# Performance work log

Hardware: AMD Instinct MI355X
Metric: run time of the kernel (lower is better)

## Reference

```python
import jax, jax.numpy as jnp
import numpy as np

B, S, H, F = 4, 1024, 768, 3072
EC, EU = 4, 4          # common / unique expert counts
CAP_FACTOR = 1.0       # common_ffn_capacity


def setup_inputs() -> dict:
    key = jax.random.key(0)
    ks = jax.random.split(key, 8)
    def w(k, shape, s=0.02):
        return jax.random.normal(k, shape, jnp.float32) * s
    return {
        "hidden_states": jax.random.normal(ks[0], (B, S, H), jnp.float32),
        "Wsc": w(ks[1], (H, EC)), "bsc": jnp.zeros((EC,), jnp.float32),
        "W1c": w(ks[2], (EC, H, F)), "b1c": jnp.zeros((EC, F), jnp.float32),
        "W2c": w(ks[3], (EC, F, H)), "b2c": jnp.zeros((EC, H), jnp.float32),
        "Wsu": w(ks[4], (H, EU)), "bsu": jnp.zeros((EU,), jnp.float32),
        "W1u": w(ks[5], (EU, H, F)), "b1u": jnp.zeros((EU, F), jnp.float32),
        "W2u": w(ks[6], (EU, F, H)), "b2u": jnp.zeros((EU, H), jnp.float32),
    }


def _ffn(x, W1, b1, W2, b2):
    # standard BERT FFN: dense -> exact GELU -> dense
    return jax.nn.gelu(x @ W1 + b1, approximate=False) @ W2 + b2


def _expert_mix(h, route, W1, b1, W2, b2, n_exp):
    # top-1 dispatch expressed as masked per-expert compute (loop over fixed small E)
    out = jnp.zeros_like(h)
    for e in range(n_exp):
        m = (route == e).astype(h.dtype)[:, None]
        out = out + m * _ffn(h, W1[e], b1[e], W2[e], b2[e])
    return out


def _drop_mask(route, pmax, capacity):
    # rank tokens within each expert group by router prob (descending);
    # tokens with rank >= capacity are 'dropped' (routed to unique experts)
    N = route.shape[0]
    order = jnp.lexsort((-jax.lax.stop_gradient(pmax), route))  # primary: expert id, secondary: -prob
    rs = route[order]
    starts = jnp.searchsorted(rs, rs, side='left')              # first index of each group
    rank_sorted = jnp.arange(N) - starts
    rank = jnp.zeros((N,), jnp.int32).at[order].set(rank_sorted.astype(jnp.int32))
    return rank >= capacity


def reference(hidden_states, Wsc, bsc, W1c, b1c, W2c, b2c, Wsu, bsu, W1u, b1u, W2u, b2u):
    shp = hidden_states.shape
    h = hidden_states.reshape(-1, shp[-1])          # [N, H]
    N = h.shape[0]
    capacity = int(CAP_FACTOR * N / EC)             # static python int

    # --- common routing (top-1 + capacity dropping) ---
    pc = jax.nn.softmax(h @ Wsc + bsc, axis=-1)
    pmax_c = jnp.max(pc, axis=-1)
    route_c = jnp.argmax(pc, axis=-1)
    dropped = _drop_mask(route_c, pmax_c, capacity)

    # NOTE: original code never truncates cluster_list, so common FFN runs on ALL tokens
    scale_c = (pmax_c / jax.lax.stop_gradient(pmax_c))[:, None]   # == 1.0, grad-carrying
    common = _expert_mix(h, route_c, W1c, b1c, W2c, b2c, EC) * scale_c

    # --- unique routing (only dropped tokens contribute) ---
    pu = jax.nn.softmax(h @ Wsu + bsu, axis=-1)
    pmax_u = jnp.max(pu, axis=-1)
    route_u = jnp.argmax(pu, axis=-1)
    scale_u = (pmax_u / jax.lax.stop_gradient(pmax_u))[:, None]
    unique = _expert_mix(h, route_u, W1u, b1u, W2u, b2u, EU) * scale_u

    # dropped tokens get common + unique; kept tokens get common only
    out = common + dropped[:, None].astype(h.dtype) * unique
    return out.reshape(shp)
```

## Files before the change

kernel.cpp:

```cpp
#include <hip/hip_runtime.h>
#include <hip/hip_bf16.h>
#include <math.h>

#define NTOK 4096
#define HDIM 768
#define FDIM 3072
#define NEXP 4
#define MAXU 3072
#define MAXT 64
#define NPOS (NTOK + MAXU)
#define RSTRIDE 76

typedef __attribute__((ext_vector_type(4))) float f32x4;
typedef __attribute__((ext_vector_type(8))) short s16x8;

__device__ __forceinline__ unsigned short f2bf(float f) {
    union { float f; unsigned int u; } v; v.f = f;
    unsigned int u = v.u;
    unsigned int r = (u + 0x7fffu + ((u >> 16) & 1u)) >> 16;
    return (unsigned short)r;
}

__device__ __forceinline__ void gload_lds16(const unsigned short* g, unsigned short* l) {
    __builtin_amdgcn_global_load_lds((const __attribute__((address_space(1))) void*)g,
                                     (__attribute__((address_space(3))) void*)l, 16, 0, 0);
}

__global__ void __launch_bounds__(256) route_kernel(
    const float* __restrict__ h, const float* __restrict__ Wsc, const float* __restrict__ bsc,
    const float* __restrict__ Wsu, const float* __restrict__ bsu,
    int* __restrict__ route_c, float* __restrict__ pmax_c,
    int* __restrict__ route_u, int* __restrict__ counts)
{
    if (blockIdx.x == 0 && threadIdx.x < 8) counts[threadIdx.x] = 0;
    int tok = blockIdx.x * 4 + (threadIdx.x >> 6);
    int lane = threadIdx.x & 63;
    const float* hr = h + (size_t)tok * HDIM;
    float ac[4] = {0.f,0.f,0.f,0.f}, au[4] = {0.f,0.f,0.f,0.f};
    for (int k = lane; k < HDIM; k += 64) {
        float x = hr[k];
        const float4 wc = *(const float4*)(Wsc + k * 4);
        const float4 wu = *(const float4*)(Wsu + k * 4);
        ac[0] += x * wc.x; ac[1] += x * wc.y; ac[2] += x * wc.z; ac[3] += x * wc.w;
        au[0] += x * wu.x; au[1] += x * wu.y; au[2] += x * wu.z; au[3] += x * wu.w;
    }
    #pragma unroll
    for (int off = 32; off > 0; off >>= 1) {
        #pragma unroll
        for (int j = 0; j < 4; ++j) {
            ac[j] += __shfl_xor(ac[j], off);
            au[j] += __shfl_xor(au[j], off);
        }
    }
    if (lane == 0) {
        float lc[4], lu[4];
        #pragma unroll
        for (int j = 0; j < 4; ++j) { lc[j] = ac[j] + bsc[j]; lu[j] = au[j] + bsu[j]; }
        int bc = 0; float mc = lc[0];
        #pragma unroll
        for (int j = 1; j < 4; ++j) if (lc[j] > mc) { mc = lc[j]; bc = j; }
        float dc = 0.f;
        #pragma unroll
        for (int j = 0; j < 4; ++j) dc += expf(lc[j] - mc);
        route_c[tok] = bc; pmax_c[tok] = 1.0f / dc;
        int bu = 0; float mu = lu[0];
        #pragma unroll
        for (int j = 1; j < 4; ++j) if (lu[j] > mu) { mu = lu[j]; bu = j; }
        route_u[tok] = bu;
    }
}

__global__ void __launch_bounds__(256) rank_kernel(
    const int* __restrict__ rc, const int* __restrict__ ru,
    const float* __restrict__ pc,
    int* __restrict__ dropped, int* __restrict__ counts, int capacity)
{
    int i = blockIdx.x, t = threadIdx.x;
    int e = rc[i]; float pi = pc[i];
    int cnt = 0;
    for (int j = t; j < NTOK; j += 256) {
        if (rc[j] == e) {
            float pj = pc[j];
            if (pj > pi || (pj == pi && j < i)) cnt++;
        }
    }
    __shared__ int red[256];
    red[t] = cnt; __syncthreads();
    for (int s = 128; s > 0; s >>= 1) {
        if (t < s) red[t] += red[t+s];
        __syncthreads();
    }
    if (t == 0) {
        int d = (red[0] >= capacity) ? 1 : 0;
        dropped[i] = d;
        atomicAdd(&counts[e], 1);
        if (d) atomicAdd(&counts[4 + ru[i]], 1);
    }
}

__global__ void offsets_kernel(const int* __restrict__ counts,
                               int* __restrict__ offAll,
                               int* __restrict__ cur,
                               int* __restrict__ tab,
                               int* __restrict__ ntot)
{
    if (threadIdx.x == 0 && blockIdx.x == 0) {
        int o = 0;
        for (int e = 0; e < 8; ++e) { offAll[e] = o; o += counts[e]; }
        offAll[8] = o;
        *ntot = o;
        for (int j = 0; j < 8; ++j) cur[j] = 0;
        int t = 0;
        for (int e = 0; e < 8; ++e) {
            int nt = (counts[e] + 127) >> 7;
            for (int m = 0; m < nt && t < MAXT; ++m) { tab[t*2] = e; tab[t*2+1] = m; ++t; }
        }
        for (; t < MAXT; ++t) { tab[t*2] = -1; tab[t*2+1] = 0; }
    }
}

__global__ void __launch_bounds__(256) scatter_kernel(
    const int* __restrict__ rc, const int* __restrict__ ru, const int* __restrict__ dropped,
    const int* __restrict__ offAll, int* __restrict__ cur, int* __restrict__ perm,
    int* __restrict__ invC, int* __restrict__ invU)
{
    int i = blockIdx.x * 256 + threadIdx.x;
    if (i >= NTOK) return;
    int e = rc[i];
    int p = offAll[e] + atomicAdd(&cur[e], 1);
    perm[p] = i;
    invC[i] = p;
    if (dropped[i]) {
        int eu = 4 + ru[i];
        int q = offAll[eu] + atomicAdd(&cur[eu], 1);
        perm[q] = i;
        invU[i] = q;
    }
}

__global__ void __launch_bounds__(192) gather_kernel(
    const float* __restrict__ h, const int* __restrict__ perm,
    const int* __restrict__ ntot, unsigned short* __restrict__ Xs)
{
    int pos = blockIdx.x;
    if (pos >= *ntot) return;
    int t = threadIdx.x;
    int tok = perm[pos];
    const float4 v = *(const float4*)(h + (size_t)tok * HDIM + t * 4);
    ushort4 o;
    o.x = f2bf(v.x); o.y = f2bf(v.y); o.z = f2bf(v.z); o.w = f2bf(v.w);
    *(ushort4*)(Xs + (size_t)pos * HDIM + t * 4) = o;
}

__global__ void __launch_bounds__(256) wtrans_kernel(
    const float* __restrict__ Wc, const float* __restrict__ Wu,
    unsigned short* __restrict__ Bt, int K, int N)
{
    int z = blockIdx.z;
    const float* We = (z < 4) ? (Wc + (size_t)z * K * N)
                              : (Wu + (size_t)(z - 4) * K * N);
    unsigned short* Be = Bt + (size_t)z * N * K;
    int k0 = blockIdx.y * 64, n0 = blockIdx.x * 64;
    __shared__ float t[64][65];
    int tid = threadIdx.x;
    int rr = tid >> 4, cc = (tid & 15) * 4;
    #pragma unroll
    for (int i = 0; i < 4; ++i) {
        int row = rr + i * 16;
        const float4 v = *(const float4*)(We + (size_t)(k0 + row) * N + n0 + cc);
        t[row][cc+0] = v.x; t[row][cc+1] = v.y; t[row][cc+2] = v.z; t[row][cc+3] = v.w;
    }
    __syncthreads();
    #pragma unroll
    for (int i = 0; i < 4; ++i) {
        int n = rr + i * 16;
        ushort4 o;
        o.x = f2bf(t[cc+0][n]); o.y = f2bf(t[cc+1][n]);
        o.z = f2bf(t[cc+2][n]); o.w = f2bf(t[cc+3][n]);
        *(ushort4*)(Be + (size_t)(n0 + n) * K + k0 + cc) = o;
    }
}

__global__ void __launch_bounds__(256, 4) ffn_gemm(
    const unsigned short* __restrict__ A, const unsigned short* __restrict__ Bt,
    const float* __restrict__ biasC, const float* __restrict__ biasU,
    const int* __restrict__ offs, const int* __restrict__ tab,
    unsigned short* __restrict__ Gout, float* __restrict__ Yout,
    int K, int N, int doGelu)
{
    int e = tab[blockIdx.y * 2];
    if (e < 0) return;
    int mt = tab[blockIdx.y * 2 + 1];
    int off = offs[e];
    int cnt = offs[e + 1] - off;
    if (mt * 128 >= cnt) return;
    int nt = blockIdx.x;
    int klen = K / gridDim.z;
    int kbeg = blockIdx.z * klen, kend = kbeg + klen;

    __shared__ unsigned short lds[9728];
    unsigned short* As = lds;
    unsigned short* Bs = lds + 4096;

    int tid = threadIdx.x;
    int lane = tid & 63, wave = tid >> 6;
    int quad = lane >> 4, l16 = lane & 15;

    f32x4 acc[2][4];
    #pragma unroll
    for (int a = 0; a < 2; ++a)
        #pragma unroll
        for (int b = 0; b < 4; ++b)
            acc[a][b] = (f32x4){0.f, 0.f, 0.f, 0.f};

    int r0 = tid >> 2, s0 = tid & 3;
    int r1 = (tid + 256) >> 2;
    int seg0 = (s0 ^ ((r0 & 3) ^ ((r0 >> 2) & 3))) * 8;
    int seg1 = (s0 ^ ((r1 & 3) ^ ((r1 >> 2) & 3))) * 8;
    int ar0 = mt * 128 + r0; if (ar0 >= cnt) ar0 = cnt - 1;
    int ar1 = mt * 128 + r1; if (ar1 >= cnt) ar1 = cnt - 1;

    const unsigned short* Ae = A + (size_t)off * K;
    const unsigned short* Be = Bt + ((size_t)e * N + (size_t)nt * 64) * K;
    const unsigned short* asrc0 = Ae + (size_t)ar0 * K + seg0;
    const unsigned short* asrc1 = Ae + (size_t)ar1 * K + seg1;
    const unsigned short* bsrc0 = Be + (size_t)r0 * K + seg0;
    unsigned short* al0 = &As[wave * 512];
    unsigned short* al1 = &As[2048 + wave * 512];
    unsigned short* bl0 = &Bs[wave * 512];
    int cca = quad ^ ((l16 & 3) ^ ((l16 >> 2) & 3));

    for (int k0 = kbeg; k0 < kend; k0 += 32) {
        gload_lds16(asrc0 + k0, al0);
        gload_lds16(asrc1 + k0, al1);
        gload_lds16(bsrc0 + k0, bl0);
        __syncthreads();

        s16x8 af[2], bf[4];
        #pragma unroll
        for (int mi = 0; mi < 2; ++mi)
            af[mi] = *(const s16x8*)&As[(wave * 32 + mi * 16 + l16) * 32 + cca * 8];
        #pragma unroll
        for (int ni = 0; ni < 4; ++ni)
            bf[ni] = *(const s16x8*)&Bs[(ni * 16 + l16) * 32 + cca * 8];
        #pragma unroll
        for (int mi = 0; mi < 2; ++mi)
            #pragma unroll
            for (int ni = 0; ni < 4; ++ni)
                acc[mi][ni] = __builtin_amdgcn_mfma_f32_16x16x32_bf16(af[mi], bf[ni], acc[mi][ni], 0, 0, 0);
        __syncthreads();
    }

    const float* bias = (e < 4) ? (biasC + (size_t)e * N) : (biasU + (size_t)(e - 4) * N);

    if (doGelu) {
        unsigned short* R = lds + wave * (32 * RSTRIDE);
        #pragma unroll
        for (int ni = 0; ni < 4; ++ni) {
            float bv = bias[nt * 64 + ni * 16 + l16];
            #pragma unroll
            for (int mi = 0; mi < 2; ++mi) {
                #pragma unroll
                for (int r = 0; r < 4; ++r) {
                    float x = acc[mi][ni][r] + bv;
                    x = 0.5f * x * (1.0f + erff(x * 0.70710678118654752440f));
                    R[(mi * 16 + quad * 4 + r) * RSTRIDE + ni * 16 + l16] = f2bf(x);
                }
            }
        }
        __builtin_amdgcn_s_waitcnt(0);
        int lrow = lane >> 4, lcol = (lane & 15) * 4;
        #pragma unroll
        for (int p = 0; p < 8; ++p) {
            int row = p * 4 + lrow;
            int gr = mt * 128 + wave * 32 + row;
            if (gr < cnt) {
                ushort4 v = *(const ushort4*)&R[row * RSTRIDE + lcol];
                *(ushort4*)&Gout[(size_t)(off + gr) * N + nt * 64 + lcol] = v;
            }
        }
    } else {
        float* Yz = Yout + (size_t)blockIdx.z * NPOS * N;
        #pragma unroll
        for (int ni = 0; ni < 4; ++ni) {
            int col = nt * 64 + ni * 16 + l16;
            float bv = (blockIdx.z == 0) ? bias[col] : 0.f;
            #pragma unroll
            for (int mi = 0; mi < 2; ++mi) {
                #pragma unroll
                for (int r = 0; r < 4; ++r) {
                    int lm = mt * 128 + wave * 32 + mi * 16 + quad * 4 + r;
                    if (lm < cnt)
                        Yz[(size_t)(off + lm) * N + col] = acc[mi][ni][r] + bv;
                }
            }
        }
    }
}

__global__ void __launch_bounds__(192) combine_kernel(
    const float* __restrict__ Y, const int* __restrict__ invC,
    const int* __restrict__ invU, const int* __restrict__ dropped,
    float* __restrict__ out)
{
    int tok = blockIdx.x, t = threadIdx.x;
    const float* Y0 = Y;
    const float* Y1 = Y + (size_t)NPOS * HDIM;
    int pc = invC[tok];
    float4 a = *(const float4*)(Y0 + (size_t)pc * HDIM + t * 4);
    float4 b = *(const float4*)(Y1 + (size_t)pc * HDIM + t * 4);
    float4 o;
    o.x = a.x + b.x; o.y = a.y + b.y; o.z = a.z + b.z; o.w = a.w + b.w;
    if (dropped[tok]) {
        int pu = invU[tok];
        float4 c = *(const float4*)(Y0 + (size_t)pu * HDIM + t * 4);
        float4 d = *(const float4*)(Y1 + (size_t)pu * HDIM + t * 4);
        o.x += c.x + d.x; o.y += c.y + d.y; o.z += c.z + d.z; o.w += c.w + d.w;
    }
    *(float4*)(out + (size_t)tok * HDIM + t * 4) = o;
}

extern "C" void kernel_launch(void* const* d_in, const int* in_sizes, int n_in,
                              void* d_out, int out_size, void* d_ws, size_t ws_size,
                              hipStream_t stream) {
    (void)in_sizes; (void)n_in; (void)out_size; (void)ws_size;
    const float* h   = (const float*)d_in[0];
    const float* Wsc = (const float*)d_in[1];
    const float* bsc = (const float*)d_in[2];
    const float* W1c = (const float*)d_in[3];
    const float* b1c = (const float*)d_in[4];
    const float* W2c = (const float*)d_in[5];
    const float* b2c = (const float*)d_in[6];
    const float* Wsu = (const float*)d_in[7];
    const float* bsu = (const float*)d_in[8];
    const float* W1u = (const float*)d_in[9];
    const float* b1u = (const float*)d_in[10];
    const float* W2u = (const float*)d_in[11];
    const float* b2u = (const float*)d_in[12];
    float* out = (float*)d_out;

    char* w = (char*)d_ws;
    size_t o = 0;
    auto carve = [&](size_t bytes) -> char* {
        char* p = w + o; o += (bytes + 255) & ~(size_t)255; return p;
    };
    int*   route_c = (int*)carve(NTOK * 4);
    float* pmax_c  = (float*)carve(NTOK * 4);
    int*   route_u = (int*)carve(NTOK * 4);
    int*   dropped = (int*)carve(NTOK * 4);
    int*   counts  = (int*)carve(8 * 4);
    int*   offAll  = (int*)carve(9 * 4);
    int*   cur     = (int*)carve(8 * 4);
    int*   ntot    = (int*)carve(4);
    int*   perm    = (int*)carve(NPOS * 4);
    int*   invC    = (int*)carve(NTOK * 4);
    int*   invU    = (int*)carve(NTOK * 4);
    int*   tab     = (int*)carve(MAXT * 2 * 4);
    unsigned short* X   = (unsigned short*)carve((size_t)NPOS * HDIM * 2);
    unsigned short* G   = (unsigned short*)carve((size_t)NPOS * FDIM * 2);
    float*          Y2  = (float*)carve((size_t)2 * NPOS * HDIM * 4);
    unsigned short* BtA = (unsigned short*)carve((size_t)8 * HDIM * FDIM * 2);
    unsigned short* BtB = (unsigned short*)carve((size_t)8 * FDIM * HDIM * 2);

    int capacity = NTOK / NEXP;

    route_kernel<<<NTOK/4, 256, 0, stream>>>(h, Wsc, bsc, Wsu, bsu,
                                             route_c, pmax_c, route_u, counts);
    rank_kernel<<<NTOK, 256, 0, stream>>>(route_c, route_u, pmax_c,
                                          dropped, counts, capacity);
    offsets_kernel<<<1, 64, 0, stream>>>(counts, offAll, cur, tab, ntot);
    scatter_kernel<<<NTOK/256, 256, 0, stream>>>(route_c, route_u, dropped,
                                                 offAll, cur, perm, invC, invU);
    gather_kernel<<<NPOS, 192, 0, stream>>>(h, perm, ntot, X);

    wtrans_kernel<<<dim3(FDIM/64, HDIM/64, 8), 256, 0, stream>>>(W1c, W1u, BtA, HDIM, FDIM);
    wtrans_kernel<<<dim3(HDIM/64, FDIM/64, 8), 256, 0, stream>>>(W2c, W2u, BtB, FDIM, HDIM);

    ffn_gemm<<<dim3(FDIM/64, MAXT, 1), 256, 0, stream>>>(
        X, BtA, b1c, b1u, offAll, tab, G, nullptr, HDIM, FDIM, 1);
    ffn_gemm<<<dim3(HDIM/64, MAXT, 2), 256, 0, stream>>>(
        G, BtB, b2c, b2u, offAll, tab, nullptr, Y2, FDIM, HDIM, 0);
    combine_kernel<<<NTOK, 192, 0, stream>>>(Y2, invC, invU, dropped, out);
}
```

Measured before the change: 410.9 us.

## Deepen GEMM K-tile to 64, widen weight transpose tiles, wave-level rank reduction

```diff
diff --git a/kernel.cpp b/kernel.cpp
--- a/kernel.cpp
+++ b/kernel.cpp
@@ -75,23 +75,20 @@
     const float* __restrict__ pc,
     int* __restrict__ dropped, int* __restrict__ counts, int capacity)
 {
-    int i = blockIdx.x, t = threadIdx.x;
+    int wave = threadIdx.x >> 6, lane = threadIdx.x & 63;
+    int i = blockIdx.x * 4 + wave;
     int e = rc[i]; float pi = pc[i];
     int cnt = 0;
-    for (int j = t; j < NTOK; j += 256) {
+    for (int j = lane; j < NTOK; j += 64) {
         if (rc[j] == e) {
             float pj = pc[j];
             if (pj > pi || (pj == pi && j < i)) cnt++;
         }
     }
-    __shared__ int red[256];
-    red[t] = cnt; __syncthreads();
-    for (int s = 128; s > 0; s >>= 1) {
-        if (t < s) red[t] += red[t+s];
-        __syncthreads();
-    }
-    if (t == 0) {
-        int d = (red[0] >= capacity) ? 1 : 0;
+    #pragma unroll
+    for (int off = 32; off > 0; off >>= 1) cnt += __shfl_xor(cnt, off);
+    if (lane == 0) {
+        int d = (cnt >= capacity) ? 1 : 0;
         dropped[i] = d;
         atomicAdd(&counts[e], 1);
         if (d) atomicAdd(&counts[4 + ru[i]], 1);
@@ -160,24 +157,25 @@
     const float* We = (z < 4) ? (Wc + (size_t)z * K * N)
                               : (Wu + (size_t)(z - 4) * K * N);
     unsigned short* Be = Bt + (size_t)z * N * K;
-    int k0 = blockIdx.y * 64, n0 = blockIdx.x * 64;
-    __shared__ float t[64][65];
+    int k0 = blockIdx.y * 128, n0 = blockIdx.x * 64;
+    __shared__ float t[128][65];
     int tid = threadIdx.x;
-    int rr = tid >> 4, cc = (tid & 15) * 4;
-    #pragma unroll
-    for (int i = 0; i < 4; ++i) {
+    int rr = tid >> 4, c4 = (tid & 15) * 4;
+    #pragma unroll
+    for (int i = 0; i < 8; ++i) {
         int row = rr + i * 16;
-        const float4 v = *(const float4*)(We + (size_t)(k0 + row) * N + n0 + cc);
-        t[row][cc+0] = v.x; t[row][cc+1] = v.y; t[row][cc+2] = v.z; t[row][cc+3] = v.w;
+        const float4 v = *(const float4*)(We + (size_t)(k0 + row) * N + n0 + c4);
+        t[row][c4+0] = v.x; t[row][c4+1] = v.y; t[row][c4+2] = v.z; t[row][c4+3] = v.w;
     }
     __syncthreads();
     #pragma unroll
-    for (int i = 0; i < 4; ++i) {
-        int n = rr + i * 16;
+    for (int i = 0; i < 8; ++i) {
+        int idx = tid + i * 256;
+        int n = idx >> 5, kk = (idx & 31) * 4;
         ushort4 o;
-        o.x = f2bf(t[cc+0][n]); o.y = f2bf(t[cc+1][n]);
-        o.z = f2bf(t[cc+2][n]); o.w = f2bf(t[cc+3][n]);
-        *(ushort4*)(Be + (size_t)(n0 + n) * K + k0 + cc) = o;
+        o.x = f2bf(t[kk+0][n]); o.y = f2bf(t[kk+1][n]);
+        o.z = f2bf(t[kk+2][n]); o.w = f2bf(t[kk+3][n]);
+        *(ushort4*)(Be + (size_t)(n0 + n) * K + k0 + kk) = o;
     }
 }
 
@@ -196,11 +194,11 @@
     if (mt * 128 >= cnt) return;
     int nt = blockIdx.x;
     int klen = K / gridDim.z;
-    int kbeg = blockIdx.z * klen, kend = kbeg + klen;
-
-    __shared__ unsigned short lds[9728];
+    int kbeg = blockIdx.z * klen;
+
+    __shared__ unsigned short lds[12288];
     unsigned short* As = lds;
-    unsigned short* Bs = lds + 4096;
+    unsigned short* Bs = lds + 8192;
 
     int tid = threadIdx.x;
     int lane = tid & 63, wave = tid >> 6;
@@ -213,41 +211,52 @@
         for (int b = 0; b < 4; ++b)
             acc[a][b] = (f32x4){0.f, 0.f, 0.f, 0.f};
 
-    int r0 = tid >> 2, s0 = tid & 3;
-    int r1 = (tid + 256) >> 2;
-    int seg0 = (s0 ^ ((r0 & 3) ^ ((r0 >> 2) & 3))) * 8;
-    int seg1 = (s0 ^ ((r1 & 3) ^ ((r1 >> 2) & 3))) * 8;
-    int ar0 = mt * 128 + r0; if (ar0 >= cnt) ar0 = cnt - 1;
-    int ar1 = mt * 128 + r1; if (ar1 >= cnt) ar1 = cnt - 1;
-
     const unsigned short* Ae = A + (size_t)off * K;
     const unsigned short* Be = Bt + ((size_t)e * N + (size_t)nt * 64) * K;
-    const unsigned short* asrc0 = Ae + (size_t)ar0 * K + seg0;
-    const unsigned short* asrc1 = Ae + (size_t)ar1 * K + seg1;
-    const unsigned short* bsrc0 = Be + (size_t)r0 * K + seg0;
-    unsigned short* al0 = &As[wave * 512];
-    unsigned short* al1 = &As[2048 + wave * 512];
-    unsigned short* bl0 = &Bs[wave * 512];
-    int cca = quad ^ ((l16 & 3) ^ ((l16 >> 2) & 3));
-
-    for (int k0 = kbeg; k0 < kend; k0 += 32) {
-        gload_lds16(asrc0 + k0, al0);
-        gload_lds16(asrc1 + k0, al1);
-        gload_lds16(bsrc0 + k0, bl0);
+
+    const unsigned short* asrc[4]; unsigned short* adst[4];
+    #pragma unroll
+    for (int j = 0; j < 4; ++j) {
+        int c = tid + j * 256;
+        int row = c >> 3, s = c & 7;
+        int gseg = (s ^ (row & 7)) * 8;
+        int ar = mt * 128 + row; if (ar >= cnt) ar = cnt - 1;
+        asrc[j] = Ae + (size_t)ar * K + kbeg + gseg;
+        adst[j] = &As[(j * 256 + wave * 64) * 8];
+    }
+    const unsigned short* bsrc[2]; unsigned short* bdst[2];
+    #pragma unroll
+    for (int j = 0; j < 2; ++j) {
+        int c = tid + j * 256;
+        int row = c >> 3, s = c & 7;
+        int gseg = (s ^ (row & 7)) * 8;
+        bsrc[j] = Be + (size_t)row * K + kbeg + gseg;
+        bdst[j] = &Bs[(j * 256 + wave * 64) * 8];
+    }
+
+    for (int k0 = 0; k0 < klen; k0 += 64) {
+        #pragma unroll
+        for (int j = 0; j < 4; ++j) gload_lds16(asrc[j] + k0, adst[j]);
+        #pragma unroll
+        for (int j = 0; j < 2; ++j) gload_lds16(bsrc[j] + k0, bdst[j]);
         __syncthreads();
 
-        s16x8 af[2], bf[4];
-        #pragma unroll
-        for (int mi = 0; mi < 2; ++mi)
-            af[mi] = *(const s16x8*)&As[(wave * 32 + mi * 16 + l16) * 32 + cca * 8];
-        #pragma unroll
-        for (int ni = 0; ni < 4; ++ni)
-            bf[ni] = *(const s16x8*)&Bs[(ni * 16 + l16) * 32 + cca * 8];
-        #pragma unroll
-        for (int mi = 0; mi < 2; ++mi)
+        #pragma unroll
+        for (int ks = 0; ks < 2; ++ks) {
+            int cc = ((ks * 4 + quad) ^ (l16 & 7)) * 8;
+            s16x8 af[2], bf[4];
+            #pragma unroll
+            for (int mi = 0; mi < 2; ++mi)
+                af[mi] = *(const s16x8*)&As[(wave * 32 + mi * 16 + l16) * 64 + cc];
             #pragma unroll
             for (int ni = 0; ni < 4; ++ni)
-                acc[mi][ni] = __builtin_amdgcn_mfma_f32_16x16x32_bf16(af[mi], bf[ni], acc[mi][ni], 0, 0, 0);
+                bf[ni] = *(const s16x8*)&Bs[(ni * 16 + l16) * 64 + cc];
+            #pragma unroll
+            for (int mi = 0; mi < 2; ++mi)
+                #pragma unroll
+                for (int ni = 0; ni < 4; ++ni)
+                    acc[mi][ni] = __builtin_amdgcn_mfma_f32_16x16x32_bf16(af[mi], bf[ni], acc[mi][ni], 0, 0, 0);
+        }
         __syncthreads();
     }
 
@@ -366,15 +375,15 @@
 
     route_kernel<<<NTOK/4, 256, 0, stream>>>(h, Wsc, bsc, Wsu, bsu,
                                              route_c, pmax_c, route_u, counts);
-    rank_kernel<<<NTOK, 256, 0, stream>>>(route_c, route_u, pmax_c,
-                                          dropped, counts, capacity);
+    rank_kernel<<<NTOK/4, 256, 0, stream>>>(route_c, route_u, pmax_c,
+                                            dropped, counts, capacity);
     offsets_kernel<<<1, 64, 0, stream>>>(counts, offAll, cur, tab, ntot);
     scatter_kernel<<<NTOK/256, 256, 0, stream>>>(route_c, route_u, dropped,
                                                  offAll, cur, perm, invC, invU);
     gather_kernel<<<NPOS, 192, 0, stream>>>(h, perm, ntot, X);
 
-    wtrans_kernel<<<dim3(FDIM/64, HDIM/64, 8), 256, 0, stream>>>(W1c, W1u, BtA, HDIM, FDIM);
-    wtrans_kernel<<<dim3(HDIM/64, FDIM/64, 8), 256, 0, stream>>>(W2c, W2u, BtB, FDIM, HDIM);
+    wtrans_kernel<<<dim3(FDIM/64, HDIM/128, 8), 256, 0, stream>>>(W1c, W1u, BtA, HDIM, FDIM);
+    wtrans_kernel<<<dim3(HDIM/64, FDIM/128, 8), 256, 0, stream>>>(W2c, W2u, BtB, FDIM, HDIM);
 
     ffn_gemm<<<dim3(FDIM/64, MAXT, 1), 256, 0, stream>>>(
         X, BtA, b1c, b1u, offAll, tab, G, nullptr, HDIM, FDIM, 1);
```

After: 405.0 us. Within noise of the previous version (-1.4%).
